# Kernel optimization log

Measured on AMD Instinct MI355X. Metric: run time of the kernel, lower is better.

The kernel has to match this reference:

```python
import jax, jax.numpy as jnp
import numpy as np

N_NODES = 100000
N_EDGES = 1600000
IN_CH = 64
HID = 128
OUT_CH = 2
N_GRAPHS = 512
LN_EPS = 1e-5


def setup_inputs() -> dict:
    key = jax.random.key(0)
    ks = jax.random.split(key, 16)
    x = jax.random.normal(ks[0], (N_NODES, IN_CH), dtype=jnp.float32)
    edge_index = jax.random.randint(ks[1], (2, N_EDGES), 0, N_NODES, dtype=jnp.int64)
    batch = jnp.sort(jax.random.randint(ks[2], (N_NODES,), 0, N_GRAPHS, dtype=jnp.int64))

    def lin(k, fan_in, fan_out):
        bound = 1.0 / np.sqrt(fan_in)
        return jax.random.uniform(k, (fan_in, fan_out), jnp.float32, -bound, bound)

    inp = {"x": x, "edge_index": edge_index, "batch": batch}
    # SAGEConv 0: in->hid; SAGEConv 1,2: hid->hid
    inp["Wl0"] = lin(ks[3], IN_CH, HID); inp["bl0"] = jnp.zeros((HID,), jnp.float32)
    inp["Wr0"] = lin(ks[4], IN_CH, HID)
    inp["Wl1"] = lin(ks[5], HID, HID); inp["bl1"] = jnp.zeros((HID,), jnp.float32)
    inp["Wr1"] = lin(ks[6], HID, HID)
    inp["Wl2"] = lin(ks[7], HID, HID); inp["bl2"] = jnp.zeros((HID,), jnp.float32)
    inp["Wr2"] = lin(ks[8], HID, HID)
    # decode: LayerNorm(hid) + Linear(hid, out)
    inp["ln_g"] = jnp.ones((HID,), jnp.float32)
    inp["ln_b"] = jnp.zeros((HID,), jnp.float32)
    inp["Wd"] = lin(ks[9], HID, OUT_CH)
    inp["bd"] = jnp.zeros((OUT_CH,), jnp.float32)
    return inp


def _sage_conv(x, src, dst, Wl, bl, Wr):
    # mean aggregation of source features onto destination nodes
    s = jax.ops.segment_sum(x[src], dst, num_segments=N_NODES)  # [N, F]
    cnt = jax.ops.segment_sum(jnp.ones((src.shape[0],), x.dtype), dst, num_segments=N_NODES)
    agg = s / jnp.maximum(cnt, 1.0)[:, None]
    return agg @ Wl + bl + x @ Wr


def reference(x, edge_index, batch, Wl0, bl0, Wr0, Wl1, bl1, Wr1, Wl2, bl2, Wr2, ln_g, ln_b, Wd, bd):
    src, dst = edge_index[0], edge_index[1]
    h = jax.nn.relu(_sage_conv(x, src, dst, Wl0, bl0, Wr0))
    h = jax.nn.relu(_sage_conv(h, src, dst, Wl1, bl1, Wr1))
    h = jax.nn.relu(_sage_conv(h, src, dst, Wl2, bl2, Wr2))
    # global_add_pool
    g = jax.ops.segment_sum(h, batch, num_segments=N_GRAPHS)  # [G, HID]
    # decode: LayerNorm + Linear
    mu = jnp.mean(g, axis=-1, keepdims=True)
    var = jnp.mean(jnp.square(g - mu), axis=-1, keepdims=True)
    gn = (g - mu) * jax.lax.rsqrt(var + LN_EPS) * ln_g + ln_b
    return gn @ Wd + bd
```

## Files before the change

kernel.cpp:

```cpp
#include <hip/hip_runtime.h>

#define N_NODES  100000
#define N_EDGES  1600000
#define N_GRAPHS 512
#define LN_EPS   1e-5f

#define NB    256
#define NPB   391
#define BCAP  8192
#define PCHUNK 8192
#define PBLOCKS ((N_EDGES + PCHUNK - 1) / PCHUNK)
#define POOL_CHUNK 64
#define POOL_BLOCKS ((N_NODES + POOL_CHUNK - 1) / POOL_CHUNK)

typedef unsigned short u16;
typedef unsigned int   u32;
typedef __attribute__((ext_vector_type(8))) short bf16x8;
typedef __attribute__((ext_vector_type(4))) float f32x4;

__device__ __forceinline__ float b2f(u16 v) {
    u32 u = ((u32)v) << 16;
    return __builtin_bit_cast(float, u);
}
__device__ __forceinline__ u16 f2b(float f) {
    u32 u = __builtin_bit_cast(u32, f);
    u32 r = (u + 0x7fffu + ((u >> 16) & 1u)) >> 16;
    return (u16)r;
}


__global__ __launch_bounds__(256)
void partition_edges(const int* __restrict__ src, const int* __restrict__ dst,
                     int* __restrict__ bcnt, uint2* __restrict__ bpool) {
    __shared__ int hist[NB];
    __shared__ int gbase[NB];
    __shared__ int cur[NB];
    int t = threadIdx.x;
    int e0 = blockIdx.x * PCHUNK;
    int e1 = e0 + PCHUNK; if (e1 > N_EDGES) e1 = N_EDGES;

    hist[t] = 0;
    __syncthreads();
    for (int e = e0 + t; e < e1; e += 256)
        atomicAdd(&hist[dst[e] / NPB], 1);
    __syncthreads();
    int h = hist[t];
    gbase[t] = (h > 0) ? atomicAdd(&bcnt[t], h) : 0;
    cur[t] = 0;
    __syncthreads();
    for (int e = e0 + t; e < e1; e += 256) {
        int d = dst[e], s = src[e];
        int b = d / NPB;
        int p = atomicAdd(&cur[b], 1);
        bpool[(size_t)b * BCAP + gbase[b] + p] = make_uint2((u32)d, (u32)s);
    }
}

__global__ void scan_buckets(const int* __restrict__ bcnt, int* __restrict__ bbase,
                             int* __restrict__ offsets) {
    __shared__ int sh[NB];
    int t = threadIdx.x;
    int v = bcnt[t];
    sh[t] = v; __syncthreads();
    for (int off = 1; off < NB; off <<= 1) {
        int add = (t >= off) ? sh[t - off] : 0;
        __syncthreads();
        sh[t] += add;
        __syncthreads();
    }
    bbase[t] = sh[t] - v;
    if (t == NB - 1) offsets[N_NODES] = sh[t];
}

__global__ __launch_bounds__(256)
void build_csr_bucket(const int* __restrict__ bcnt, const int* __restrict__ bbase,
                      const uint2* __restrict__ bpool,
                      int* __restrict__ offsets, int* __restrict__ csr) {
    __shared__ int sA[512];
    __shared__ int sB[512];
    __shared__ int csrL[BCAP];
    int b = blockIdx.x, t = threadIdx.x;
    int nlo = b * NPB;
    int NL = N_NODES - nlo; if (NL > NPB) NL = NPB;
    int count = bcnt[b], base = bbase[b];
    const uint2* pool = bpool + (size_t)b * BCAP;

    sA[t] = 0; sA[t + 256] = 0;
    __syncthreads();
    for (int i = t; i < count; i += 256)
        atomicAdd(&sA[(int)pool[i].x - nlo], 1);
    __syncthreads();
    int c0 = sA[t], c1 = sA[t + 256];

    int* a = sA; int* c = sB;
    for (int off = 1; off < 512; off <<= 1) {
        c[t]       = a[t]       + ((t >= off)       ? a[t - off]       : 0);
        c[t + 256] = a[t + 256] + ((t + 256 >= off) ? a[t + 256 - off] : 0);
        __syncthreads();
        int* tmp = a; a = c; c = tmp;
    }
    int ex0 = a[t] - c0, ex1 = a[t + 256] - c1;
    if (t < NL)       offsets[nlo + t]       = base + ex0;
    if (t + 256 < NL) offsets[nlo + t + 256] = base + ex1;
    c[t] = ex0; c[t + 256] = ex1;
    __syncthreads();
    for (int i = t; i < count; i += 256) {
        uint2 p = pool[i];
        int pos = atomicAdd(&c[(int)p.x - nlo], 1);
        csrL[pos] = (int)p.y;
    }
    __syncthreads();
    for (int i = t; i < count; i += 256)
        csr[base + i] = csrL[i];
}


__global__ __launch_bounds__(256)
void conv_f32_bf16(const float* __restrict__ in, u16* __restrict__ out, int n4) {
    int i = blockIdx.x * 256 + threadIdx.x;
    if (i < n4) {
        float4 v = ((const float4*)in)[i];
        u32 lo = (u32)f2b(v.x) | ((u32)f2b(v.y) << 16);
        u32 hi = (u32)f2b(v.z) | ((u32)f2b(v.w) << 16);
        ((uint2*)out)[i] = make_uint2(lo, hi);
    }
}

__global__ __launch_bounds__(256)
void conv_weights(const float* __restrict__ Wl, const float* __restrict__ Wr,
                  int K1, int KC, u16* __restrict__ Wt) {
    int idx = blockIdx.x * 256 + threadIdx.x;
    if (idx >= 128 * KC) return;
    int c = idx / KC, k = idx % KC;
    float v = (k < K1) ? Wl[k * 128 + c] : Wr[(k - K1) * 128 + c];
    Wt[idx] = f2b(v);
}


template<int F>
__global__ __launch_bounds__(256)
void aggregate_bf16(const u16* __restrict__ in, const int* __restrict__ offsets,
                    const int* __restrict__ csr, u16* __restrict__ out) {
    int grp = threadIdx.x >> 5;
    int sub = threadIdx.x & 31;
    int n = blockIdx.x * 8 + grp;
    int o0 = offsets[n], o1 = offsets[n + 1];
    int d = o1 - o0;
    float inv = 1.0f / (float)(d > 1 ? d : 1);

    if (F == 128) {
        const uint2* base = (const uint2*)in;
        float acc[4][4];
        #pragma unroll
        for (int j = 0; j < 4; j++)
            #pragma unroll
            for (int c = 0; c < 4; c++) acc[j][c] = 0.f;

        int o = o0;
        for (; o + 4 <= o1; o += 4) {
            int s0 = csr[o + 0], s1 = csr[o + 1], s2 = csr[o + 2], s3 = csr[o + 3];
            uint2 v0 = base[(size_t)s0 * 32 + sub];
            uint2 v1 = base[(size_t)s1 * 32 + sub];
            uint2 v2 = base[(size_t)s2 * 32 + sub];
            uint2 v3 = base[(size_t)s3 * 32 + sub];
            acc[0][0] += b2f((u16)(v0.x & 0xffffu)); acc[0][1] += b2f((u16)(v0.x >> 16));
            acc[0][2] += b2f((u16)(v0.y & 0xffffu)); acc[0][3] += b2f((u16)(v0.y >> 16));
            acc[1][0] += b2f((u16)(v1.x & 0xffffu)); acc[1][1] += b2f((u16)(v1.x >> 16));
            acc[1][2] += b2f((u16)(v1.y & 0xffffu)); acc[1][3] += b2f((u16)(v1.y >> 16));
            acc[2][0] += b2f((u16)(v2.x & 0xffffu)); acc[2][1] += b2f((u16)(v2.x >> 16));
            acc[2][2] += b2f((u16)(v2.y & 0xffffu)); acc[2][3] += b2f((u16)(v2.y >> 16));
            acc[3][0] += b2f((u16)(v3.x & 0xffffu)); acc[3][1] += b2f((u16)(v3.x >> 16));
            acc[3][2] += b2f((u16)(v3.y & 0xffffu)); acc[3][3] += b2f((u16)(v3.y >> 16));
        }
        for (; o < o1; o++) {
            int s = csr[o];
            uint2 v = base[(size_t)s * 32 + sub];
            acc[0][0] += b2f((u16)(v.x & 0xffffu)); acc[0][1] += b2f((u16)(v.x >> 16));
            acc[0][2] += b2f((u16)(v.y & 0xffffu)); acc[0][3] += b2f((u16)(v.y >> 16));
        }
        float r0 = ((acc[0][0] + acc[1][0]) + (acc[2][0] + acc[3][0])) * inv;
        float r1 = ((acc[0][1] + acc[1][1]) + (acc[2][1] + acc[3][1])) * inv;
        float r2 = ((acc[0][2] + acc[1][2]) + (acc[2][2] + acc[3][2])) * inv;
        float r3 = ((acc[0][3] + acc[1][3]) + (acc[2][3] + acc[3][3])) * inv;
        uint2 w;
        w.x = (u32)f2b(r0) | ((u32)f2b(r1) << 16);
        w.y = (u32)f2b(r2) | ((u32)f2b(r3) << 16);
        ((uint2*)out)[(size_t)n * 32 + sub] = w;
    } else {
        const u32* base = (const u32*)in;
        float acc[4][2];
        #pragma unroll
        for (int j = 0; j < 4; j++) { acc[j][0] = 0.f; acc[j][1] = 0.f; }

        int o = o0;
        for (; o + 4 <= o1; o += 4) {
            int s0 = csr[o + 0], s1 = csr[o + 1], s2 = csr[o + 2], s3 = csr[o + 3];
            u32 v0 = base[(size_t)s0 * 32 + sub];
            u32 v1 = base[(size_t)s1 * 32 + sub];
            u32 v2 = base[(size_t)s2 * 32 + sub];
            u32 v3 = base[(size_t)s3 * 32 + sub];
            acc[0][0] += b2f((u16)(v0 & 0xffffu)); acc[0][1] += b2f((u16)(v0 >> 16));
            acc[1][0] += b2f((u16)(v1 & 0xffffu)); acc[1][1] += b2f((u16)(v1 >> 16));
            acc[2][0] += b2f((u16)(v2 & 0xffffu)); acc[2][1] += b2f((u16)(v2 >> 16));
            acc[3][0] += b2f((u16)(v3 & 0xffffu)); acc[3][1] += b2f((u16)(v3 >> 16));
        }
        for (; o < o1; o++) {
            int s = csr[o];
            u32 v = base[(size_t)s * 32 + sub];
            acc[0][0] += b2f((u16)(v & 0xffffu)); acc[0][1] += b2f((u16)(v >> 16));
        }
        float r0 = ((acc[0][0] + acc[1][0]) + (acc[2][0] + acc[3][0])) * inv;
        float r1 = ((acc[0][1] + acc[1][1]) + (acc[2][1] + acc[3][1])) * inv;
        ((u32*)out)[(size_t)n * 32 + sub] = (u32)f2b(r0) | ((u32)f2b(r1) << 16);
    }
}


template<int KHALF>
__global__ __launch_bounds__(256)
void gemm_mfma(const u16* __restrict__ A1, const u16* __restrict__ A2,
               const u16* __restrict__ Wt, const float* __restrict__ bias,
               u16* __restrict__ out) {
    constexpr int KC    = 2 * KHALF;
    constexpr int NKS   = KC / 32;
    constexpr int RB    = KHALF * 2;
    constexpr int C16   = RB / 16;
    constexpr int TILEB = 64 * RB;
    constexpr int ITER  = (TILEB / 16) / 256;

    __shared__ __align__(16) char lds_t[2 * TILEB];

    int t = threadIdx.x;
    int lane = t & 63, w = t >> 6;
    int l15 = lane & 15, l4 = lane >> 4;
    int mbase = blockIdx.x * 64;

    {
        const char* Ab0 = (const char*)(A1 + (size_t)mbase * KHALF);
        const char* Ab1 = (const char*)(A2 + (size_t)mbase * KHALF);
        #pragma unroll
        for (int tl = 0; tl < 2; tl++) {
            const char* Ab = tl ? Ab1 : Ab0;
            #pragma unroll
            for (int i = 0; i < ITER; i++) {
                int q = i * 256 + t;
                int row = q / C16;
                int c16 = q % C16;
                int c16s = c16 ^ (row & 7);
                uint4 v = make_uint4(0u, 0u, 0u, 0u);
                if (mbase + row < N_NODES)
                    v = *(const uint4*)(Ab + (size_t)row * RB + (size_t)c16 * 16);
                *(uint4*)&lds_t[tl * TILEB + row * RB + c16s * 16] = v;
            }
        }
    }

    bf16x8 bfr[2][NKS];
    #pragma unroll
    for (int ct = 0; ct < 2; ct++)
        #pragma unroll
        for (int ks = 0; ks < NKS; ks++) {
            int row = w * 32 + ct * 16 + l15;
            int kb  = ks * 32 + l4 * 8;
            bfr[ct][ks] = *reinterpret_cast<const bf16x8*>(Wt + row * KC + kb);
        }

    f32x4 acc[4][2];
    #pragma unroll
    for (int i = 0; i < 4; i++)
        #pragma unroll
        for (int j = 0; j < 2; j++)
            acc[i][j] = (f32x4){0.f, 0.f, 0.f, 0.f};

    __syncthreads();

    #pragma unroll
    for (int ks = 0; ks < NKS; ks++) {
        int tl  = (ks < NKS / 2) ? 0 : 1;
        int ksl = (ks < NKS / 2) ? ks : (ks - NKS / 2);
        bf16x8 afr[4];
        #pragma unroll
        for (int rt = 0; rt < 4; rt++) {
            int rl = rt * 16 + l15;
            int c16 = ksl * 4 + l4;
            int c16s = c16 ^ (rl & 7);
            afr[rt] = *reinterpret_cast<const bf16x8*>(
                &lds_t[tl * TILEB + rl * RB + c16s * 16]);
        }
        #pragma unroll
        for (int rt = 0; rt < 4; rt++)
            #pragma unroll
            for (int ct = 0; ct < 2; ct++)
                acc[rt][ct] = __builtin_amdgcn_mfma_f32_16x16x32_bf16(
                    afr[rt], bfr[ct][ks], acc[rt][ct], 0, 0, 0);
    }

    #pragma unroll
    for (int ct = 0; ct < 2; ct++) {
        int col = w * 32 + ct * 16 + l15;
        float bv = bias[col];
        #pragma unroll
        for (int rt = 0; rt < 4; rt++) {
            #pragma unroll
            for (int j = 0; j < 4; j++) {
                int row = mbase + rt * 16 + l4 * 4 + j;
                if (row < N_NODES) {
                    float v = fmaxf(acc[rt][ct][j] + bv, 0.f);
                    out[(size_t)row * 128 + col] = f2b(v);
                }
            }
        }
    }
}


__global__ __launch_bounds__(128)
void pool_partial(const u16* __restrict__ h, const int* __restrict__ batch,
                  float* __restrict__ gpool) {
    int c = threadIdx.x;
    int n0 = blockIdx.x * POOL_CHUNK;
    int n1 = n0 + POOL_CHUNK; if (n1 > N_NODES) n1 = N_NODES;
    float run = 0.f;
    int curg = -1;
    for (int r = n0; r < n1; r++) {
        int gid = batch[r];
        if (gid != curg) {
            if (curg >= 0) atomicAdd(&gpool[curg * 128 + c], run);
            run = 0.f; curg = gid;
        }
        run += b2f(h[(size_t)r * 128 + c]);
    }
    if (curg >= 0) atomicAdd(&gpool[curg * 128 + c], run);
}

__global__ __launch_bounds__(64)
void ln_decode(const float* __restrict__ gpool,
               const float* __restrict__ ln_g, const float* __restrict__ ln_b,
               const float* __restrict__ Wd, const float* __restrict__ bd,
               float* __restrict__ out) {
    int g = blockIdx.x, lane = threadIdx.x;
    float v0 = gpool[g * 128 + lane];
    float v1 = gpool[g * 128 + 64 + lane];
    float s = v0 + v1;
    #pragma unroll
    for (int off = 32; off > 0; off >>= 1) s += __shfl_xor(s, off, 64);
    float mu = s * (1.0f / 128.f);
    float d0 = v0 - mu, d1 = v1 - mu;
    float q = d0 * d0 + d1 * d1;
    #pragma unroll
    for (int off = 32; off > 0; off >>= 1) q += __shfl_xor(q, off, 64);
    float rs = rsqrtf(q * (1.0f / 128.f) + LN_EPS);
    float gn0 = d0 * rs * ln_g[lane]      + ln_b[lane];
    float gn1 = d1 * rs * ln_g[64 + lane] + ln_b[64 + lane];
    float o0 = gn0 * Wd[lane * 2 + 0] + gn1 * Wd[(64 + lane) * 2 + 0];
    float o1 = gn0 * Wd[lane * 2 + 1] + gn1 * Wd[(64 + lane) * 2 + 1];
    #pragma unroll
    for (int off = 32; off > 0; off >>= 1) {
        o0 += __shfl_xor(o0, off, 64);
        o1 += __shfl_xor(o1, off, 64);
    }
    if (lane == 0) {
        out[g * 2 + 0] = o0 + bd[0];
        out[g * 2 + 1] = o1 + bd[1];
    }
}


extern "C" void kernel_launch(void* const* d_in, const int* in_sizes, int n_in,
                              void* d_out, int out_size, void* d_ws, size_t ws_size,
                              hipStream_t stream) {
    (void)in_sizes; (void)n_in; (void)out_size; (void)ws_size;

    const float* x     = (const float*)d_in[0];
    const int*   ei    = (const int*)d_in[1];
    const int*   batch = (const int*)d_in[2];
    const float* Wl0 = (const float*)d_in[3];
    const float* bl0 = (const float*)d_in[4];
    const float* Wr0 = (const float*)d_in[5];
    const float* Wl1 = (const float*)d_in[6];
    const float* bl1 = (const float*)d_in[7];
    const float* Wr1 = (const float*)d_in[8];
    const float* Wl2 = (const float*)d_in[9];
    const float* bl2 = (const float*)d_in[10];
    const float* Wr2 = (const float*)d_in[11];
    const float* ln_g = (const float*)d_in[12];
    const float* ln_b = (const float*)d_in[13];
    const float* Wd  = (const float*)d_in[14];
    const float* bd  = (const float*)d_in[15];
    float* out = (float*)d_out;

    const int* src = ei;
    const int* dst = ei + N_EDGES;

    char* ws = (char*)d_ws;
    int*   csr     = (int*)(ws + 0);
    int*   offsets = (int*)(ws + 6400000);
    int*   bcnt    = (int*)(ws + 6800128);
    int*   bbase   = (int*)(ws + 6801152);
    uint2* bpool   = (uint2*)(ws + 6802176);
    u16*   x16     = (u16*)(ws + 23579392);
    u16*   aggbuf  = (u16*)(ws + 36379392);
    u16*   bufB    = (u16*)(ws + 61979392);
    u16*   bufC    = (u16*)(ws + 87579392);
    u16*   Wt0     = (u16*)(ws + 113179392);
    u16*   Wt1     = (u16*)(ws + 113212160);
    u16*   Wt2     = (u16*)(ws + 113277696);
    float* gpool   = (float*)(ws + 113343232);

    hipMemsetAsync(bcnt, 0, NB * sizeof(int), stream);
    hipMemsetAsync(gpool, 0, N_GRAPHS * 128 * sizeof(float), stream);

    partition_edges<<<PBLOCKS, 256, 0, stream>>>(src, dst, bcnt, bpool);
    scan_buckets<<<1, 256, 0, stream>>>(bcnt, bbase, offsets);
    build_csr_bucket<<<NB, 256, 0, stream>>>(bcnt, bbase, bpool, offsets, csr);

    conv_f32_bf16<<<(N_NODES * 64 / 4 + 255) / 256, 256, 0, stream>>>(x, x16, N_NODES * 64 / 4);
    conv_weights<<<(128 * 128 + 255) / 256, 256, 0, stream>>>(Wl0, Wr0, 64, 128, Wt0);
    conv_weights<<<(128 * 256 + 255) / 256, 256, 0, stream>>>(Wl1, Wr1, 128, 256, Wt1);
    conv_weights<<<(128 * 256 + 255) / 256, 256, 0, stream>>>(Wl2, Wr2, 128, 256, Wt2);

    const int aggGrid  = N_NODES / 8;
    const int gemmGrid = (N_NODES + 63) / 64;

    aggregate_bf16<64><<<aggGrid, 256, 0, stream>>>(x16, offsets, csr, aggbuf);
    gemm_mfma<64><<<gemmGrid, 256, 0, stream>>>(aggbuf, x16, Wt0, bl0, bufB);
    aggregate_bf16<128><<<aggGrid, 256, 0, stream>>>(bufB, offsets, csr, aggbuf);
    gemm_mfma<128><<<gemmGrid, 256, 0, stream>>>(aggbuf, bufB, Wt1, bl1, bufC);
    aggregate_bf16<128><<<aggGrid, 256, 0, stream>>>(bufC, offsets, csr, aggbuf);
    gemm_mfma<128><<<gemmGrid, 256, 0, stream>>>(aggbuf, bufC, Wt2, bl2, bufB);

    pool_partial<<<POOL_BLOCKS, 128, 0, stream>>>(bufB, batch, gpool);
    ln_decode<<<N_GRAPHS, 64, 0, stream>>>(gpool, ln_g, ln_b, Wd, bd, out);
}
```

Baseline: 340.9 us.

## Fuse setup kernels, pack bucket entries to 32 bits, widen pool loads

Replaces the two memsets with one zero-init kernel, folds the bucket scan into each CSR-build block, and merges the x conversion and three weight-conversion kernels into one launch. Bucket pool entries are packed as a 17-bit source plus a local destination index in one u32, which halves pool traffic. Pooling now reads two bf16 values per thread with 256-thread blocks. The aim is fewer launches and less memory traffic, at the cost of a redundant per-block scan and a packing that assumes node ids fit in 17 bits.

New measurement: 340.6 us. About the same (-0.1%).

```diff
diff --git a/kernel.cpp b/kernel.cpp
--- a/kernel.cpp
+++ b/kernel.cpp
@@ -10,8 +10,8 @@
 #define BCAP  8192
 #define PCHUNK 8192
 #define PBLOCKS ((N_EDGES + PCHUNK - 1) / PCHUNK)
-#define POOL_CHUNK 64
-#define POOL_BLOCKS ((N_NODES + POOL_CHUNK - 1) / POOL_CHUNK)
+#define POOL_NPB 256
+#define POOL_BLOCKS ((N_NODES + POOL_NPB - 1) / POOL_NPB)
 
 typedef unsigned short u16;
 typedef unsigned int   u32;
@@ -29,9 +29,16 @@
 }
 
 
+__global__ void zero_init(int* __restrict__ bcnt, float* __restrict__ gpool) {
+    int b = blockIdx.x, t = threadIdx.x;
+    if (b < 256) gpool[b * 256 + t] = 0.f;
+    else bcnt[t] = 0;
+}
+
+
 __global__ __launch_bounds__(256)
 void partition_edges(const int* __restrict__ src, const int* __restrict__ dst,
-                     int* __restrict__ bcnt, uint2* __restrict__ bpool) {
+                     int* __restrict__ bcnt, u32* __restrict__ bpool) {
     __shared__ int hist[NB];
     __shared__ int gbase[NB];
     __shared__ int cur[NB];
@@ -50,49 +57,46 @@
     __syncthreads();
     for (int e = e0 + t; e < e1; e += 256) {
         int d = dst[e], s = src[e];
-        int b = d / NPB;
-        int p = atomicAdd(&cur[b], 1);
-        bpool[(size_t)b * BCAP + gbase[b] + p] = make_uint2((u32)d, (u32)s);
-    }
-}
-
-__global__ void scan_buckets(const int* __restrict__ bcnt, int* __restrict__ bbase,
-                             int* __restrict__ offsets) {
-    __shared__ int sh[NB];
-    int t = threadIdx.x;
-    int v = bcnt[t];
-    sh[t] = v; __syncthreads();
-    for (int off = 1; off < NB; off <<= 1) {
-        int add = (t >= off) ? sh[t - off] : 0;
-        __syncthreads();
-        sh[t] += add;
-        __syncthreads();
-    }
-    bbase[t] = sh[t] - v;
-    if (t == NB - 1) offsets[N_NODES] = sh[t];
-}
-
-__global__ __launch_bounds__(256)
-void build_csr_bucket(const int* __restrict__ bcnt, const int* __restrict__ bbase,
-                      const uint2* __restrict__ bpool,
+        int bk = d / NPB;
+        int p = atomicAdd(&cur[bk], 1);
+        bpool[(size_t)bk * BCAP + gbase[bk] + p] =
+            ((u32)(d - bk * NPB) << 17) | (u32)s;
+    }
+}
+
+__global__ __launch_bounds__(256)
+void build_csr_bucket(const int* __restrict__ bcnt, const u32* __restrict__ bpool,
                       int* __restrict__ offsets, int* __restrict__ csr) {
     __shared__ int sA[512];
     __shared__ int sB[512];
     __shared__ int csrL[BCAP];
     int b = blockIdx.x, t = threadIdx.x;
+
+    sA[t] = bcnt[t];
+    __syncthreads();
+    int* a = sA; int* c = sB;
+    for (int off = 1; off < 256; off <<= 1) {
+        c[t] = a[t] + ((t >= off) ? a[t - off] : 0);
+        __syncthreads();
+        int* tmp = a; a = c; c = tmp;
+    }
+    int count = bcnt[b];
+    int base  = a[b] - count;
+    if (b == NB - 1 && t == 0) offsets[N_NODES] = a[NB - 1];
+    __syncthreads();
+
     int nlo = b * NPB;
     int NL = N_NODES - nlo; if (NL > NPB) NL = NPB;
-    int count = bcnt[b], base = bbase[b];
-    const uint2* pool = bpool + (size_t)b * BCAP;
+    const u32* pool = bpool + (size_t)b * BCAP;
 
     sA[t] = 0; sA[t + 256] = 0;
     __syncthreads();
     for (int i = t; i < count; i += 256)
-        atomicAdd(&sA[(int)pool[i].x - nlo], 1);
+        atomicAdd(&sA[(int)(pool[i] >> 17)], 1);
     __syncthreads();
     int c0 = sA[t], c1 = sA[t + 256];
 
-    int* a = sA; int* c = sB;
+    a = sA; c = sB;
     for (int off = 1; off < 512; off <<= 1) {
         c[t]       = a[t]       + ((t >= off)       ? a[t - off]       : 0);
         c[t + 256] = a[t + 256] + ((t + 256 >= off) ? a[t + 256 - off] : 0);
@@ -105,9 +109,9 @@
     c[t] = ex0; c[t + 256] = ex1;
     __syncthreads();
     for (int i = t; i < count; i += 256) {
-        uint2 p = pool[i];
-        int pos = atomicAdd(&c[(int)p.x - nlo], 1);
-        csrL[pos] = (int)p.y;
+        u32 p = pool[i];
+        int pos = atomicAdd(&c[(int)(p >> 17)], 1);
+        csrL[pos] = (int)(p & 0x1FFFFu);
     }
     __syncthreads();
     for (int i = t; i < count; i += 256)
@@ -116,24 +120,35 @@
 
 
 __global__ __launch_bounds__(256)
-void conv_f32_bf16(const float* __restrict__ in, u16* __restrict__ out, int n4) {
-    int i = blockIdx.x * 256 + threadIdx.x;
-    if (i < n4) {
-        float4 v = ((const float4*)in)[i];
+void conv_all(const float* __restrict__ x,
+              const float* __restrict__ Wl0, const float* __restrict__ Wr0,
+              const float* __restrict__ Wl1, const float* __restrict__ Wr1,
+              const float* __restrict__ Wl2, const float* __restrict__ Wr2,
+              u16* __restrict__ x16, u16* __restrict__ Wt0,
+              u16* __restrict__ Wt1, u16* __restrict__ Wt2) {
+    int b = blockIdx.x, t = threadIdx.x;
+    if (b < 6250) {
+        int i = b * 256 + t;
+        float4 v = ((const float4*)x)[i];
         u32 lo = (u32)f2b(v.x) | ((u32)f2b(v.y) << 16);
         u32 hi = (u32)f2b(v.z) | ((u32)f2b(v.w) << 16);
-        ((uint2*)out)[i] = make_uint2(lo, hi);
-    }
-}
-
-__global__ __launch_bounds__(256)
-void conv_weights(const float* __restrict__ Wl, const float* __restrict__ Wr,
-                  int K1, int KC, u16* __restrict__ Wt) {
-    int idx = blockIdx.x * 256 + threadIdx.x;
-    if (idx >= 128 * KC) return;
-    int c = idx / KC, k = idx % KC;
-    float v = (k < K1) ? Wl[k * 128 + c] : Wr[(k - K1) * 128 + c];
-    Wt[idx] = f2b(v);
+        ((uint2*)x16)[i] = make_uint2(lo, hi);
+    } else if (b < 6250 + 64) {
+        int idx = (b - 6250) * 256 + t;
+        int ch = idx / 128, k = idx % 128;
+        float v = (k < 64) ? Wl0[k * 128 + ch] : Wr0[(k - 64) * 128 + ch];
+        Wt0[idx] = f2b(v);
+    } else if (b < 6250 + 64 + 128) {
+        int idx = (b - 6314) * 256 + t;
+        int ch = idx / 256, k = idx % 256;
+        float v = (k < 128) ? Wl1[k * 128 + ch] : Wr1[(k - 128) * 128 + ch];
+        Wt1[idx] = f2b(v);
+    } else {
+        int idx = (b - 6442) * 256 + t;
+        int ch = idx / 256, k = idx % 256;
+        float v = (k < 128) ? Wl2[k * 128 + ch] : Wr2[(k - 128) * 128 + ch];
+        Wt2[idx] = f2b(v);
+    }
 }
 
 
@@ -314,23 +329,33 @@
 }
 
 
-__global__ __launch_bounds__(128)
+__global__ __launch_bounds__(256)
 void pool_partial(const u16* __restrict__ h, const int* __restrict__ batch,
                   float* __restrict__ gpool) {
-    int c = threadIdx.x;
-    int n0 = blockIdx.x * POOL_CHUNK;
-    int n1 = n0 + POOL_CHUNK; if (n1 > N_NODES) n1 = N_NODES;
-    float run = 0.f;
+    int grp = threadIdx.x >> 6;
+    int c   = threadIdx.x & 63;
+    int n0 = blockIdx.x * POOL_NPB + grp * 64;
+    int n1 = n0 + 64; if (n1 > N_NODES) n1 = N_NODES;
+    const u32* h32 = (const u32*)h;
+    float r0 = 0.f, r1 = 0.f;
     int curg = -1;
     for (int r = n0; r < n1; r++) {
         int gid = batch[r];
         if (gid != curg) {
-            if (curg >= 0) atomicAdd(&gpool[curg * 128 + c], run);
-            run = 0.f; curg = gid;
-        }
-        run += b2f(h[(size_t)r * 128 + c]);
-    }
-    if (curg >= 0) atomicAdd(&gpool[curg * 128 + c], run);
+            if (curg >= 0) {
+                atomicAdd(&gpool[curg * 128 + c * 2 + 0], r0);
+                atomicAdd(&gpool[curg * 128 + c * 2 + 1], r1);
+            }
+            r0 = 0.f; r1 = 0.f; curg = gid;
+        }
+        u32 v = h32[(size_t)r * 64 + c];
+        r0 += b2f((u16)(v & 0xffffu));
+        r1 += b2f((u16)(v >> 16));
+    }
+    if (curg >= 0) {
+        atomicAdd(&gpool[curg * 128 + c * 2 + 0], r0);
+        atomicAdd(&gpool[curg * 128 + c * 2 + 1], r1);
+    }
 }
 
 __global__ __launch_bounds__(64)
@@ -396,28 +421,21 @@
     int*   csr     = (int*)(ws + 0);
     int*   offsets = (int*)(ws + 6400000);
     int*   bcnt    = (int*)(ws + 6800128);
-    int*   bbase   = (int*)(ws + 6801152);
-    uint2* bpool   = (uint2*)(ws + 6802176);
-    u16*   x16     = (u16*)(ws + 23579392);
-    u16*   aggbuf  = (u16*)(ws + 36379392);
-    u16*   bufB    = (u16*)(ws + 61979392);
-    u16*   bufC    = (u16*)(ws + 87579392);
-    u16*   Wt0     = (u16*)(ws + 113179392);
-    u16*   Wt1     = (u16*)(ws + 113212160);
-    u16*   Wt2     = (u16*)(ws + 113277696);
-    float* gpool   = (float*)(ws + 113343232);
-
-    hipMemsetAsync(bcnt, 0, NB * sizeof(int), stream);
-    hipMemsetAsync(gpool, 0, N_GRAPHS * 128 * sizeof(float), stream);
-
+    u32*   bpool   = (u32*)(ws + 6801152);
+    u16*   x16     = (u16*)(ws + 15189760);
+    u16*   aggbuf  = (u16*)(ws + 27989760);
+    u16*   bufB    = (u16*)(ws + 53589760);
+    u16*   bufC    = (u16*)(ws + 79189760);
+    u16*   Wt0     = (u16*)(ws + 104789760);
+    u16*   Wt1     = (u16*)(ws + 104822528);
+    u16*   Wt2     = (u16*)(ws + 104888064);
+    float* gpool   = (float*)(ws + 104953600);
+
+    zero_init<<<257, 256, 0, stream>>>(bcnt, gpool);
     partition_edges<<<PBLOCKS, 256, 0, stream>>>(src, dst, bcnt, bpool);
-    scan_buckets<<<1, 256, 0, stream>>>(bcnt, bbase, offsets);
-    build_csr_bucket<<<NB, 256, 0, stream>>>(bcnt, bbase, bpool, offsets, csr);
-
-    conv_f32_bf16<<<(N_NODES * 64 / 4 + 255) / 256, 256, 0, stream>>>(x, x16, N_NODES * 64 / 4);
-    conv_weights<<<(128 * 128 + 255) / 256, 256, 0, stream>>>(Wl0, Wr0, 64, 128, Wt0);
-    conv_weights<<<(128 * 256 + 255) / 256, 256, 0, stream>>>(Wl1, Wr1, 128, 256, Wt1);
-    conv_weights<<<(128 * 256 + 255) / 256, 256, 0, stream>>>(Wl2, Wr2, 128, 256, Wt2);
+    build_csr_bucket<<<NB, 256, 0, stream>>>(bcnt, bpool, offsets, csr);
+    conv_all<<<6570, 256, 0, stream>>>(x, Wl0, Wr0, Wl1, Wr1, Wl2, Wr2,
+                                       x16, Wt0, Wt1, Wt2);
 
     const int aggGrid  = N_NODES / 8;
     const int gemmGrid = (N_NODES + 63) / 64;
@@ -429,6 +447,6 @@
     aggregate_bf16<128><<<aggGrid, 256, 0, stream>>>(bufC, offsets, csr, aggbuf);
     gemm_mfma<128><<<gemmGrid, 256, 0, stream>>>(aggbuf, bufC, Wt2, bl2, bufB);
 
-    pool_partial<<<POOL_BLOCKS, 128, 0, stream>>>(bufB, batch, gpool);
+    pool_partial<<<POOL_BLOCKS, 256, 0, stream>>>(bufB, batch, gpool);
     ln_decode<<<N_GRAPHS, 64, 0, stream>>>(gpool, ln_g, ln_b, Wd, bd, out);
 }
```
